# Kernel optimization log

Hardware: AMD Instinct MI355X
Metric: run time of the kernel (lower is better)

Reference implementation:

```python
import jax, jax.numpy as jnp
import numpy as np

EMBED_DIM = 512
N_QUERY = 4096
N_PROTO = 1024


def setup_inputs() -> dict:
    key = jax.random.key(0)
    k_q, k_p, k_wmu = jax.random.split(key, 3)
    d = EMBED_DIM
    bound = (6.0 / (d + d)) ** 0.5
    return {
        "query_features": jax.random.normal(k_q, (N_QUERY, d), dtype=jnp.float32),
        "prototypes": jax.random.normal(k_p, (N_PROTO, d), dtype=jnp.float32),
        "weight_mu": jax.random.uniform(k_wmu, (d, d), dtype=jnp.float32, minval=-bound, maxval=bound),
        "weight_rho": jnp.full((d, d), -3.0, dtype=jnp.float32),
        "bias_mu": jnp.zeros((d,), dtype=jnp.float32),
        "bias_rho": jnp.full((d,), 0.01, dtype=jnp.float32),
        "n_samples": 10,
    }


def reference(query_features, prototypes, weight_mu, weight_rho, bias_mu, bias_rho, n_samples):
    d = weight_mu.shape[0]
    # softplus reparameterization (same each iteration in the original loop)
    weight_sigma = jnp.log1p(jnp.exp(weight_rho))  # [d, d]
    bias_sigma = jnp.log1p(jnp.exp(bias_rho))      # [d]
    # batched MC weight/bias samples: [S, d, d] and [S, d]
    key = jax.random.key(42)
    kw, kb = jax.random.split(key)
    eps_w = jax.random.normal(kw, (n_samples, d, d), dtype=weight_mu.dtype)
    eps_b = jax.random.normal(kb, (n_samples, d), dtype=bias_mu.dtype)
    w = weight_mu[None] + weight_sigma[None] * eps_w   # [S, d, d]
    b = bias_mu[None] + bias_sigma[None] * eps_b       # [S, d]
    # F.linear(x, W_sample.T, b) == x @ W_sample + b
    tq = jnp.einsum('qd,sde->sqe', query_features, w) + b[:, None, :]  # [S, Q, d]
    # cdist via ||a||^2 + ||b||^2 - 2 a.b
    sq_q = jnp.sum(tq * tq, axis=-1)                    # [S, Q]
    sq_p = jnp.sum(prototypes * prototypes, axis=-1)    # [P]
    cross = jnp.einsum('sqe,pe->sqp', tq, prototypes)   # [S, Q, P]
    sqd = sq_q[:, :, None] + sq_p[None, None, :] - 2.0 * cross
    dists = jnp.sqrt(jnp.maximum(sqd, 1e-12))           # [S, Q, P]
    mean_distance = jnp.mean(dists, axis=0)
    uncertainty = jnp.std(dists, axis=0, ddof=1)        # torch.std is unbiased
    return mean_distance, uncertainty
```

## Files before the change

kernel.cpp:

```cpp
#include <hip/hip_runtime.h>
#include <stdint.h>

#define NS 10
#define DIM 512
#define NQ 4096
#define NP 1024

typedef unsigned short ushort_t;
typedef __bf16 bf16el_t;
typedef bf16el_t bf16x8 __attribute__((ext_vector_type(8)));
typedef float floatx4 __attribute__((ext_vector_type(4)));

__host__ __device__ __forceinline__ uint32_t rotl32(uint32_t x, int r) {
  return (x << r) | (x >> (32 - r));
}

__host__ __device__ __forceinline__ void threefry2x32(uint32_t k0, uint32_t k1,
                                                      uint32_t x0, uint32_t x1,
                                                      uint32_t* o0, uint32_t* o1) {
  uint32_t ks2 = k0 ^ k1 ^ 0x1BD11BDAu;
  x0 += k0; x1 += k1;
#define TF_R(r) { x0 += x1; x1 = rotl32(x1, r); x1 ^= x0; }
  TF_R(13) TF_R(15) TF_R(26) TF_R(6)   x0 += k1;  x1 += ks2 + 1u;
  TF_R(17) TF_R(29) TF_R(16) TF_R(24)  x0 += ks2; x1 += k0 + 2u;
  TF_R(13) TF_R(15) TF_R(26) TF_R(6)   x0 += k0;  x1 += k1 + 3u;
  TF_R(17) TF_R(29) TF_R(16) TF_R(24)  x0 += k1;  x1 += ks2 + 4u;
  TF_R(13) TF_R(15) TF_R(26) TF_R(6)   x0 += ks2; x1 += k0 + 5u;
#undef TF_R
  *o0 = x0; *o1 = x1;
}

__device__ __forceinline__ uint32_t jax_random_bits(uint32_t k0, uint32_t k1, uint32_t idx) {
  uint32_t o0, o1;
  threefry2x32(k0, k1, 0u, idx, &o0, &o1);
  return o0 ^ o1;
}

__device__ __forceinline__ float erfinvf_xla(float x) {
  float w = -log1pf(-x * x);
  float p;
  if (w < 5.0f) {
    w -= 2.5f;
    p = 2.81022636e-08f;
    p = fmaf(p, w, 3.43273939e-07f);
    p = fmaf(p, w, -3.5233877e-06f);
    p = fmaf(p, w, -4.39150654e-06f);
    p = fmaf(p, w, 0.00021858087f);
    p = fmaf(p, w, -0.00125372503f);
    p = fmaf(p, w, -0.00417768164f);
    p = fmaf(p, w, 0.246640727f);
    p = fmaf(p, w, 1.50140941f);
  } else {
    w = sqrtf(w) - 3.0f;
    p = -0.000200214257f;
    p = fmaf(p, w, 0.000100950558f);
    p = fmaf(p, w, 0.00134934322f);
    p = fmaf(p, w, -0.00367342844f);
    p = fmaf(p, w, 0.00573950773f);
    p = fmaf(p, w, -0.0076224613f);
    p = fmaf(p, w, 0.00943887047f);
    p = fmaf(p, w, 1.00167406f);
    p = fmaf(p, w, 2.83297682f);
  }
  return p * x;
}

__device__ __forceinline__ float jax_bits_to_normal(uint32_t bits) {
  float f = __uint_as_float((bits >> 9) | 0x3F800000u) - 1.0f;
  float u = f * 2.0f - 0.99999994f;
  u = fmaxf(u, -0.99999994f);
  return 1.41421356f * erfinvf_xla(u);
}

__device__ __forceinline__ float softplusf(float x) { return log1pf(expf(x)); }

__device__ __forceinline__ float bf2f(ushort_t u) {
  return __uint_as_float(((uint32_t)u) << 16);
}
__device__ __forceinline__ ushort_t f2bf(float f) {
  uint32_t u = __float_as_uint(f);
  u += 0x7FFFu + ((u >> 16) & 1u);
  return (ushort_t)(u >> 16);
}

__device__ __forceinline__ void gll16(const void* g, void* l) {
  __builtin_amdgcn_global_load_lds(
      (const __attribute__((address_space(1))) uint32_t*)g,
      (__attribute__((address_space(3))) uint32_t*)l, 16, 0, 0);
}

__global__ __launch_bounds__(256) void gen_w_kernel(const float* __restrict__ wmu,
                                                    const float* __restrict__ wrho,
                                                    ushort_t* __restrict__ wt,
                                                    uint32_t kw0, uint32_t kw1) {
  uint32_t tid = blockIdx.x * 256u + threadIdx.x;
  uint32_t s = tid >> 18;
  uint32_t r = tid & 0x3FFFFu;
  uint32_t e = r >> 9;
  uint32_t k = r & 511u;
  uint32_t eps_idx = (s << 18) | (k << 9) | e;
  uint32_t bits = jax_random_bits(kw0, kw1, eps_idx);
  float n = jax_bits_to_normal(bits);
  uint32_t mi = (k << 9) | e;
  float w = wmu[mi] + softplusf(wrho[mi]) * n;
  wt[tid] = f2bf(w);
}

__global__ __launch_bounds__(256) void prep_kernel(const float* __restrict__ qf,
                                                   const float* __restrict__ pf,
                                                   const float* __restrict__ bmu,
                                                   const float* __restrict__ brho,
                                                   ushort_t* __restrict__ qb,
                                                   ushort_t* __restrict__ pb,
                                                   float* __restrict__ sqp,
                                                   float* __restrict__ bvec,
                                                   float* __restrict__ sqq,
                                                   uint32_t kb0, uint32_t kb1) {
  const int blk = blockIdx.x;
  const int tid = threadIdx.x;
  if (blk < 2048) {
    int i = (blk * 256 + tid) * 4;
    float4 v = *(const float4*)&qf[i];
    uint2 r;
    r.x = (uint32_t)f2bf(v.x) | ((uint32_t)f2bf(v.y) << 16);
    r.y = (uint32_t)f2bf(v.z) | ((uint32_t)f2bf(v.w) << 16);
    *(uint2*)&qb[i] = r;
  } else if (blk < 2304) {
    int p = (blk - 2048) * 4 + (tid >> 6);
    int lane = tid & 63;
    const float* src = pf + p * DIM + lane * 8;
    float4 a = *(const float4*)src;
    float4 b = *(const float4*)(src + 4);
    float vals[8] = {a.x, a.y, a.z, a.w, b.x, b.y, b.z, b.w};
    ushort_t o[8];
    float ss = 0.f;
#pragma unroll
    for (int i = 0; i < 8; ++i) {
      o[i] = f2bf(vals[i]);
      float f = bf2f(o[i]);
      ss += f * f;
    }
    *(uint4*)&pb[p * DIM + lane * 8] = *(const uint4*)o;
#pragma unroll
    for (int off = 32; off; off >>= 1) ss += __shfl_xor(ss, off, 64);
    if (lane == 0) sqp[p] = ss;
  } else if (blk < 2324) {
    uint32_t t2 = (blk - 2304) * 256u + tid;
    uint32_t e = t2 & 511u;
    uint32_t bits = jax_random_bits(kb0, kb1, t2);
    float n = jax_bits_to_normal(bits);
    bvec[t2] = bmu[e] + softplusf(brho[e]) * n;
  } else {
    int i = (blk - 2324) * 256 + tid;
    sqq[i] = 0.f;
  }
}

__global__ __launch_bounds__(256) void gemm_tq_kernel(const ushort_t* __restrict__ qb,
                                                      const ushort_t* __restrict__ wt,
                                                      const float* __restrict__ bvec,
                                                      ushort_t* __restrict__ tq,
                                                      float* __restrict__ sqq) {
  __shared__ __align__(16) ushort_t ls[2 * 128 * 64];
  ushort_t* lsA = ls;
  ushort_t* lsB = ls + 128 * 64;
  const int lane = threadIdx.x & 63;
  const int wave = threadIdx.x >> 6;
  const int wm = wave >> 1, wn = wave & 1;
  const int qBase = blockIdx.x * 128;
  const int eBase = blockIdx.y * 128;
  const int s = blockIdx.z;
  const ushort_t* wbase = wt + (size_t)s * (DIM * DIM);
  const int srow = lane >> 3;
  const int scol = ((lane & 7) ^ srow) * 16;
  const char* gA = (const char*)qb + (size_t)(qBase + wave * 32 + srow) * (DIM * 2) + scol;
  const char* gB = (const char*)wbase + (size_t)(eBase + wave * 32 + srow) * (DIM * 2) + scol;
  char* lA = (char*)&lsA[wave * 32 * 64];
  char* lB = (char*)&lsB[wave * 32 * 64];
  const int cn = lane & 15;
  const int cn7 = cn & 7;
  const int jc = lane >> 4;
  const floatx4 fzero = {0.f, 0.f, 0.f, 0.f};
  floatx4 acc[4][4];
#pragma unroll
  for (int mi = 0; mi < 4; ++mi)
#pragma unroll
    for (int ni = 0; ni < 4; ++ni) acc[mi][ni] = fzero;

  for (int kt = 0; kt < 8; ++kt) {
    __syncthreads();
#pragma unroll
    for (int j = 0; j < 4; ++j) {
      gll16(gA + (size_t)j * 8 * (DIM * 2), lA + j * 1024);
      gll16(gB + (size_t)j * 8 * (DIM * 2), lB + j * 1024);
    }
    gA += 128; gB += 128;
    __syncthreads();
#pragma unroll
    for (int c = 0; c < 8; c += 4) {
      const int po = ((c + jc) ^ cn7) << 3;
      bf16x8 aF[4], bF[4];
#pragma unroll
      for (int mi = 0; mi < 4; ++mi)
        aF[mi] = *(const bf16x8*)&lsA[(wm * 64 + mi * 16 + cn) * 64 + po];
#pragma unroll
      for (int ni = 0; ni < 4; ++ni)
        bF[ni] = *(const bf16x8*)&lsB[(wn * 64 + ni * 16 + cn) * 64 + po];
#pragma unroll
      for (int mi = 0; mi < 4; ++mi)
#pragma unroll
        for (int ni = 0; ni < 4; ++ni)
          acc[mi][ni] = __builtin_amdgcn_mfma_f32_16x16x32_bf16(aF[mi], bF[ni], acc[mi][ni], 0, 0, 0);
    }
  }

  __syncthreads();
  ushort_t* area = ls + wave * 4096;
  float bv[4];
#pragma unroll
  for (int ni = 0; ni < 4; ++ni) bv[ni] = bvec[s * DIM + eBase + wn * 64 + ni * 16 + cn];
  const int jc4 = jc * 4;
#pragma unroll
  for (int mi = 0; mi < 4; ++mi)
#pragma unroll
    for (int ni = 0; ni < 4; ++ni)
#pragma unroll
      for (int r = 0; r < 4; ++r) {
        const int lr = mi * 16 + jc4 + r;
        const int lc = ni * 16 + cn;
        const int off = lr * 64 + (((lc >> 3) ^ (lr & 7)) << 3) + (lc & 7);
        area[off] = f2bf(acc[mi][ni][r] + bv[ni]);
      }
  __syncthreads();
  const int rr = lane >> 3;
  const int ch = lane & 7;
  const int physc = ch ^ rr;
  const size_t tqs = (size_t)s * (NQ * DIM);
#pragma unroll
  for (int pass = 0; pass < 8; ++pass) {
    const int lr = pass * 8 + rr;
    uint4 v = *(const uint4*)&area[lr * 64 + physc * 8];
    uint32_t wsv[4] = {v.x, v.y, v.z, v.w};
    float ss = 0.f;
#pragma unroll
    for (int i = 0; i < 4; ++i) {
      float lo = bf2f((ushort_t)(wsv[i] & 0xFFFFu));
      float hi = bf2f((ushort_t)(wsv[i] >> 16));
      ss += lo * lo + hi * hi;
    }
    ss += __shfl_xor(ss, 1, 64);
    ss += __shfl_xor(ss, 2, 64);
    ss += __shfl_xor(ss, 4, 64);
    const int q = qBase + wm * 64 + lr;
    *(uint4*)&tq[tqs + (size_t)q * DIM + eBase + wn * 64 + ch * 8] = v;
    if (ch == 0) atomicAdd(&sqq[s * NQ + q], ss);
  }
}

__global__ __launch_bounds__(256) void gemm_dist_kernel(const ushort_t* __restrict__ tq,
                                                        const ushort_t* __restrict__ pb,
                                                        const float* __restrict__ sqq,
                                                        const float* __restrict__ sqp,
                                                        float* __restrict__ out) {
  __shared__ __align__(16) ushort_t lsA[64 * 128];
  __shared__ __align__(16) ushort_t lsB[128 * 128];
  const int lane = threadIdx.x & 63;
  const int wave = threadIdx.x >> 6;
  const int wm = wave >> 1;
  const int wn = wave & 1;
  const int qBase = blockIdx.x * 64;
  const int pBase = blockIdx.y * 128;
  const int srow = lane >> 4;
  const int scc = lane & 15;
  const int sccx = scc ^ srow;
  const char* gA = (const char*)tq + (size_t)(qBase + wave * 16 + srow) * (DIM * 2);
  const char* gB = (const char*)pb + (size_t)(pBase + wave * 32 + srow) * (DIM * 2);
  char* lA = (char*)lsA + wave * 4096;
  char* lB = (char*)lsB + wave * 8192;
  const int cn = lane & 15;
  const int jc = lane >> 4;
  const int rq = jc * 4;
  const floatx4 fzero = {0.f, 0.f, 0.f, 0.f};

  float sum[2][4][4] = {};
  float ssq[2][4][4] = {};
  float sqp_v[4];
#pragma unroll
  for (int ni = 0; ni < 4; ++ni) sqp_v[ni] = sqp[pBase + wn * 64 + ni * 16 + cn];

  for (int s = 0; s < NS; ++s) {
    floatx4 acc[2][4];
#pragma unroll
    for (int mi = 0; mi < 2; ++mi)
#pragma unroll
      for (int ni = 0; ni < 4; ++ni) acc[mi][ni] = fzero;

    for (int kt = 0; kt < 4; ++kt) {
      __syncthreads();
#pragma unroll
      for (int g = 0; g < 4; ++g)
        gll16(gA + (size_t)g * 4 * (DIM * 2) + ((sccx ^ (g * 4)) << 4), lA + g * 1024);
#pragma unroll
      for (int g = 0; g < 8; ++g)
        gll16(gB + (size_t)g * 4 * (DIM * 2) + ((sccx ^ ((g & 3) * 4)) << 4), lB + g * 1024);
      gA += 256; gB += 256;
      __syncthreads();
#pragma unroll
      for (int c4 = 0; c4 < 4; ++c4) {
        const int po = (((c4 * 4 + jc) ^ cn) & 15) << 3;
        bf16x8 aF[2], bF[4];
#pragma unroll
        for (int mi = 0; mi < 2; ++mi)
          aF[mi] = *(const bf16x8*)&lsA[(wm * 32 + mi * 16 + cn) * 128 + po];
#pragma unroll
        for (int ni = 0; ni < 4; ++ni)
          bF[ni] = *(const bf16x8*)&lsB[(wn * 64 + ni * 16 + cn) * 128 + po];
#pragma unroll
        for (int mi = 0; mi < 2; ++mi)
#pragma unroll
          for (int ni = 0; ni < 4; ++ni)
            acc[mi][ni] = __builtin_amdgcn_mfma_f32_16x16x32_bf16(aF[mi], bF[ni], acc[mi][ni], 0, 0, 0);
      }
    }
    gA += (size_t)NQ * DIM * 2 - 1024;
    gB -= 1024;
#pragma unroll
    for (int mi = 0; mi < 2; ++mi) {
      float4 aqv = *(const float4*)&sqq[s * NQ + qBase + wm * 32 + mi * 16 + rq];
      float aqa[4] = {aqv.x, aqv.y, aqv.z, aqv.w};
#pragma unroll
      for (int r = 0; r < 4; ++r) {
        float aq = aqa[r];
#pragma unroll
        for (int ni = 0; ni < 4; ++ni) {
          float sqd = fmaxf(fmaf(-2.0f, acc[mi][ni][r], aq + sqp_v[ni]), 1e-12f);
          sum[mi][ni][r] += sqrtf(sqd);
          ssq[mi][ni][r] += sqd;
        }
      }
    }
  }
#pragma unroll
  for (int mi = 0; mi < 2; ++mi)
#pragma unroll
    for (int ni = 0; ni < 4; ++ni)
#pragma unroll
      for (int r = 0; r < 4; ++r) {
        int q = qBase + wm * 32 + mi * 16 + rq + r;
        int p = pBase + wn * 64 + ni * 16 + cn;
        float sm = sum[mi][ni][r];
        float mean = sm * 0.1f;
        float var = (ssq[mi][ni][r] - sm * sm * 0.1f) * (1.0f / 9.0f);
        out[(size_t)q * NP + p] = mean;
        out[(size_t)NQ * NP + (size_t)q * NP + p] = sqrtf(fmaxf(var, 0.0f));
      }
}

extern "C" void kernel_launch(void* const* d_in, const int* in_sizes, int n_in,
                              void* d_out, int out_size, void* d_ws, size_t ws_size,
                              hipStream_t stream) {
  const float* qf   = (const float*)d_in[0];
  const float* pf   = (const float*)d_in[1];
  const float* wmu  = (const float*)d_in[2];
  const float* wrho = (const float*)d_in[3];
  const float* bmu  = (const float*)d_in[4];
  const float* brho = (const float*)d_in[5];
  float* out = (float*)d_out;
  char* ws = (char*)d_ws;
  ushort_t* wt   = (ushort_t*)(ws);
  ushort_t* qb   = (ushort_t*)(ws + 5242880);
  ushort_t* pb   = (ushort_t*)(ws + 9437184);
  float*    bvec = (float*)   (ws + 10485760);
  float*    sqp  = (float*)   (ws + 10506240);
  ushort_t* tq   = (ushort_t*)(ws + 10510336);
  float*    sqq  = (float*)   (ws + 52453376);

  uint32_t kw0, kw1, kb0, kb1;
  threefry2x32(0u, 42u, 0u, 0u, &kw0, &kw1);
  threefry2x32(0u, 42u, 0u, 1u, &kb0, &kb1);

  hipLaunchKernelGGL(gen_w_kernel, dim3(10240), dim3(256), 0, stream, wmu, wrho, wt, kw0, kw1);
  hipLaunchKernelGGL(prep_kernel, dim3(2484), dim3(256), 0, stream,
                     qf, pf, bmu, brho, qb, pb, sqp, bvec, sqq, kb0, kb1);
  hipLaunchKernelGGL(gemm_tq_kernel, dim3(32, 4, 10), dim3(256), 0, stream, qb, wt, bvec, tq, sqq);
  hipLaunchKernelGGL(gemm_dist_kernel, dim3(64, 8), dim3(256), 0, stream, tq, pb, sqq, sqp, out);
}
```

Measured before the change: 210.3 us.

## Restructure distance GEMM to keep all samples' accumulators and reuse prototype tiles

The distance kernel now loops over K tiles on the outside and over the 10 samples on the inside. It keeps a 64x64 output tile's accumulators for every sample in registers, so the prototype fragments are loaded from LDS once per K tile and reused across all samples. Query tiles for the next sample are prefetched into a double-buffered LDS area while the current sample's MFMAs run. The grid doubles to 64x16 blocks with smaller 64-wide prototype tiles and launch_bounds(256,2). This raises register pressure (160 accumulator floats plus 16 B fragments per thread), which risks spills or lower occupancy.

New measurement: 223.3 us. +6.2%, slower.

```diff
diff --git a/kernel.cpp b/kernel.cpp
--- a/kernel.cpp
+++ b/kernel.cpp
@@ -257,103 +257,107 @@
   }
 }
 
-__global__ __launch_bounds__(256) void gemm_dist_kernel(const ushort_t* __restrict__ tq,
-                                                        const ushort_t* __restrict__ pb,
-                                                        const float* __restrict__ sqq,
-                                                        const float* __restrict__ sqp,
-                                                        float* __restrict__ out) {
-  __shared__ __align__(16) ushort_t lsA[64 * 128];
-  __shared__ __align__(16) ushort_t lsB[128 * 128];
+__global__ __launch_bounds__(256, 2) void gemm_dist_kernel(const ushort_t* __restrict__ tq,
+                                                           const ushort_t* __restrict__ pb,
+                                                           const float* __restrict__ sqq,
+                                                           const float* __restrict__ sqp,
+                                                           float* __restrict__ out) {
+  __shared__ __align__(16) ushort_t lsB[64 * 128];
+  __shared__ __align__(16) ushort_t lsA[2 * 64 * 128];
   const int lane = threadIdx.x & 63;
   const int wave = threadIdx.x >> 6;
-  const int wm = wave >> 1;
-  const int wn = wave & 1;
   const int qBase = blockIdx.x * 64;
-  const int pBase = blockIdx.y * 128;
-  const int srow = lane >> 4;
-  const int scc = lane & 15;
-  const int sccx = scc ^ srow;
-  const char* gA = (const char*)tq + (size_t)(qBase + wave * 16 + srow) * (DIM * 2);
-  const char* gB = (const char*)pb + (size_t)(pBase + wave * 32 + srow) * (DIM * 2);
-  char* lA = (char*)lsA + wave * 4096;
-  char* lB = (char*)lsB + wave * 8192;
+  const int pBase = blockIdx.y * 64;
   const int cn = lane & 15;
   const int jc = lane >> 4;
-  const int rq = jc * 4;
+  const int xorb = cn ^ jc;
+  const size_t aRowB = (size_t)(qBase + wave * 16 + jc) * (DIM * 2);
+  const size_t pRowB = (size_t)(pBase + wave * 16 + jc) * (DIM * 2);
+  const char* tqb = (const char*)tq;
+  const char* pbb = (const char*)pb;
+  char* lAb = (char*)lsA;
+  char* lBb = (char*)lsB;
+  int po[4];
+#pragma unroll
+  for (int c4 = 0; c4 < 4; ++c4) po[c4] = ((c4 * 4 + jc) ^ cn) << 3;
   const floatx4 fzero = {0.f, 0.f, 0.f, 0.f};
-
-  float sum[2][4][4] = {};
-  float ssq[2][4][4] = {};
-  float sqp_v[4];
-#pragma unroll
-  for (int ni = 0; ni < 4; ++ni) sqp_v[ni] = sqp[pBase + wn * 64 + ni * 16 + cn];
-
-  for (int s = 0; s < NS; ++s) {
-    floatx4 acc[2][4];
-#pragma unroll
-    for (int mi = 0; mi < 2; ++mi)
-#pragma unroll
-      for (int ni = 0; ni < 4; ++ni) acc[mi][ni] = fzero;
-
-    for (int kt = 0; kt < 4; ++kt) {
-      __syncthreads();
-#pragma unroll
-      for (int g = 0; g < 4; ++g)
-        gll16(gA + (size_t)g * 4 * (DIM * 2) + ((sccx ^ (g * 4)) << 4), lA + g * 1024);
-#pragma unroll
-      for (int g = 0; g < 8; ++g)
-        gll16(gB + (size_t)g * 4 * (DIM * 2) + ((sccx ^ ((g & 3) * 4)) << 4), lB + g * 1024);
-      gA += 256; gB += 256;
-      __syncthreads();
-#pragma unroll
-      for (int c4 = 0; c4 < 4; ++c4) {
-        const int po = (((c4 * 4 + jc) ^ cn) & 15) << 3;
-        bf16x8 aF[2], bF[4];
-#pragma unroll
-        for (int mi = 0; mi < 2; ++mi)
-          aF[mi] = *(const bf16x8*)&lsA[(wm * 32 + mi * 16 + cn) * 128 + po];
-#pragma unroll
-        for (int ni = 0; ni < 4; ++ni)
-          bF[ni] = *(const bf16x8*)&lsB[(wn * 64 + ni * 16 + cn) * 128 + po];
-#pragma unroll
-        for (int mi = 0; mi < 2; ++mi)
-#pragma unroll
-          for (int ni = 0; ni < 4; ++ni)
-            acc[mi][ni] = __builtin_amdgcn_mfma_f32_16x16x32_bf16(aF[mi], bF[ni], acc[mi][ni], 0, 0, 0);
-      }
-    }
-    gA += (size_t)NQ * DIM * 2 - 1024;
-    gB -= 1024;
-#pragma unroll
-    for (int mi = 0; mi < 2; ++mi) {
-      float4 aqv = *(const float4*)&sqq[s * NQ + qBase + wm * 32 + mi * 16 + rq];
-      float aqa[4] = {aqv.x, aqv.y, aqv.z, aqv.w};
-#pragma unroll
-      for (int r = 0; r < 4; ++r) {
-        float aq = aqa[r];
-#pragma unroll
-        for (int ni = 0; ni < 4; ++ni) {
-          float sqd = fmaxf(fmaf(-2.0f, acc[mi][ni][r], aq + sqp_v[ni]), 1e-12f);
-          sum[mi][ni][r] += sqrtf(sqd);
-          ssq[mi][ni][r] += sqd;
+  floatx4 acc[NS][4];
+#pragma unroll
+  for (int s = 0; s < NS; ++s)
+#pragma unroll
+    for (int ni = 0; ni < 4; ++ni) acc[s][ni] = fzero;
+
+  for (int kt = 0; kt < 4; ++kt) {
+    const size_t kOff = (size_t)kt * 256;
+#pragma unroll
+    for (int g = 0; g < 4; ++g) {
+      const size_t gRow = (size_t)g * 4 * (DIM * 2);
+      const size_t gSw = (size_t)((xorb ^ (g * 4)) << 4);
+      gll16(pbb + pRowB + gRow + gSw + kOff, lBb + wave * 4096 + g * 1024);
+      gll16(tqb + aRowB + gRow + gSw + kOff, lAb + wave * 4096 + g * 1024);
+    }
+    __syncthreads();
+    bf16x8 bFr[16];
+#pragma unroll
+    for (int c4 = 0; c4 < 4; ++c4)
+#pragma unroll
+      for (int ni = 0; ni < 4; ++ni)
+        bFr[c4 * 4 + ni] = *(const bf16x8*)&lsB[(ni * 16 + cn) * 128 + po[c4]];
+#pragma unroll
+    for (int s = 0; s < NS; ++s) {
+      if (s < NS - 1) {
+        char* dst = lAb + ((s + 1) & 1) * 16384 + wave * 4096;
+#pragma unroll
+        for (int g = 0; g < 4; ++g) {
+          const size_t gRow = (size_t)g * 4 * (DIM * 2);
+          const size_t gSw = (size_t)((xorb ^ (g * 4)) << 4);
+          gll16(tqb + (size_t)(s + 1) * (NQ * DIM * 2) + aRowB + gRow + gSw + kOff,
+                dst + g * 1024);
         }
       }
-    }
-  }
-#pragma unroll
-  for (int mi = 0; mi < 2; ++mi)
-#pragma unroll
-    for (int ni = 0; ni < 4; ++ni)
-#pragma unroll
-      for (int r = 0; r < 4; ++r) {
-        int q = qBase + wm * 32 + mi * 16 + rq + r;
-        int p = pBase + wn * 64 + ni * 16 + cn;
-        float sm = sum[mi][ni][r];
-        float mean = sm * 0.1f;
-        float var = (ssq[mi][ni][r] - sm * sm * 0.1f) * (1.0f / 9.0f);
-        out[(size_t)q * NP + p] = mean;
-        out[(size_t)NQ * NP + (size_t)q * NP + p] = sqrtf(fmaxf(var, 0.0f));
+      const ushort_t* aBuf = lsA + (s & 1) * 8192 + (wave * 16 + cn) * 128;
+#pragma unroll
+      for (int c4 = 0; c4 < 4; ++c4) {
+        bf16x8 aF = *(const bf16x8*)&aBuf[po[c4]];
+#pragma unroll
+        for (int ni = 0; ni < 4; ++ni)
+          acc[s][ni] = __builtin_amdgcn_mfma_f32_16x16x32_bf16(aF, bFr[c4 * 4 + ni], acc[s][ni], 0, 0, 0);
       }
+      __syncthreads();
+    }
+  }
+
+  float sqp_v[4];
+#pragma unroll
+  for (int ni = 0; ni < 4; ++ni) sqp_v[ni] = sqp[pBase + ni * 16 + cn];
+  float sum[4][4] = {};
+  float ssq[4][4] = {};
+#pragma unroll
+  for (int s = 0; s < NS; ++s) {
+    float4 aqv = *(const float4*)&sqq[s * NQ + qBase + wave * 16 + jc * 4];
+    float aqa[4] = {aqv.x, aqv.y, aqv.z, aqv.w};
+#pragma unroll
+    for (int r = 0; r < 4; ++r) {
+#pragma unroll
+      for (int ni = 0; ni < 4; ++ni) {
+        float sqd = fmaxf(fmaf(-2.0f, acc[s][ni][r], aqa[r] + sqp_v[ni]), 1e-12f);
+        sum[ni][r] += sqrtf(sqd);
+        ssq[ni][r] += sqd;
+      }
+    }
+  }
+#pragma unroll
+  for (int ni = 0; ni < 4; ++ni)
+#pragma unroll
+    for (int r = 0; r < 4; ++r) {
+      const int q = qBase + wave * 16 + jc * 4 + r;
+      const int p = pBase + ni * 16 + cn;
+      float sm = sum[ni][r];
+      float mean = sm * 0.1f;
+      float var = (ssq[ni][r] - sm * sm * 0.1f) * (1.0f / 9.0f);
+      out[(size_t)q * NP + p] = mean;
+      out[(size_t)NQ * NP + (size_t)q * NP + p] = sqrtf(fmaxf(var, 0.0f));
+    }
 }
 
 extern "C" void kernel_launch(void* const* d_in, const int* in_sizes, int n_in,
@@ -383,5 +387,5 @@
   hipLaunchKernelGGL(prep_kernel, dim3(2484), dim3(256), 0, stream,
                      qf, pf, bmu, brho, qb, pb, sqp, bvec, sqq, kb0, kb1);
   hipLaunchKernelGGL(gemm_tq_kernel, dim3(32, 4, 10), dim3(256), 0, stream, qb, wt, bvec, tq, sqq);
-  hipLaunchKernelGGL(gemm_dist_kernel, dim3(64, 8), dim3(256), 0, stream, tq, pb, sqq, sqp, out);
-}
+  hipLaunchKernelGGL(gemm_dist_kernel, dim3(64, 16), dim3(256), 0, stream, tq, pb, sqq, sqp, out);
+}
```

## Merge weight generation into prep kernel, share A tile across two samples, swap dist grid

Applied to the files above, without the earlier changes.

The separate weight-sampling kernel is folded into the prep kernel, saving one launch. The tq GEMM now computes two MC samples per block, so each query tile in LDS feeds two weight tiles, halving A-tile loads and the grid depth. This doubles accumulator registers and grows LDS to three tiles, which may cut occupancy. The distance GEMM grid is transposed so adjacent blocks share the same query rows, which may improve L2 reuse of tq.

New measurement: 237.7 us. 13.0% more time.

```diff
diff --git a/kernel.cpp b/kernel.cpp
--- a/kernel.cpp
+++ b/kernel.cpp
@@ -89,44 +89,43 @@
       (__attribute__((address_space(3))) uint32_t*)l, 16, 0, 0);
 }
 
-__global__ __launch_bounds__(256) void gen_w_kernel(const float* __restrict__ wmu,
-                                                    const float* __restrict__ wrho,
-                                                    ushort_t* __restrict__ wt,
-                                                    uint32_t kw0, uint32_t kw1) {
-  uint32_t tid = blockIdx.x * 256u + threadIdx.x;
-  uint32_t s = tid >> 18;
-  uint32_t r = tid & 0x3FFFFu;
-  uint32_t e = r >> 9;
-  uint32_t k = r & 511u;
-  uint32_t eps_idx = (s << 18) | (k << 9) | e;
-  uint32_t bits = jax_random_bits(kw0, kw1, eps_idx);
-  float n = jax_bits_to_normal(bits);
-  uint32_t mi = (k << 9) | e;
-  float w = wmu[mi] + softplusf(wrho[mi]) * n;
-  wt[tid] = f2bf(w);
-}
-
 __global__ __launch_bounds__(256) void prep_kernel(const float* __restrict__ qf,
                                                    const float* __restrict__ pf,
+                                                   const float* __restrict__ wmu,
+                                                   const float* __restrict__ wrho,
                                                    const float* __restrict__ bmu,
                                                    const float* __restrict__ brho,
+                                                   ushort_t* __restrict__ wt,
                                                    ushort_t* __restrict__ qb,
                                                    ushort_t* __restrict__ pb,
                                                    float* __restrict__ sqp,
                                                    float* __restrict__ bvec,
                                                    float* __restrict__ sqq,
+                                                   uint32_t kw0, uint32_t kw1,
                                                    uint32_t kb0, uint32_t kb1) {
   const int blk = blockIdx.x;
   const int tid = threadIdx.x;
-  if (blk < 2048) {
-    int i = (blk * 256 + tid) * 4;
+  if (blk < 10240) {
+    uint32_t t = blk * 256u + tid;
+    uint32_t s = t >> 18;
+    uint32_t r = t & 0x3FFFFu;
+    uint32_t e = r >> 9;
+    uint32_t k = r & 511u;
+    uint32_t eps_idx = (s << 18) | (k << 9) | e;
+    uint32_t bits = jax_random_bits(kw0, kw1, eps_idx);
+    float n = jax_bits_to_normal(bits);
+    uint32_t mi = (k << 9) | e;
+    float w = wmu[mi] + softplusf(wrho[mi]) * n;
+    wt[t] = f2bf(w);
+  } else if (blk < 12288) {
+    int i = ((blk - 10240) * 256 + tid) * 4;
     float4 v = *(const float4*)&qf[i];
     uint2 r;
     r.x = (uint32_t)f2bf(v.x) | ((uint32_t)f2bf(v.y) << 16);
     r.y = (uint32_t)f2bf(v.z) | ((uint32_t)f2bf(v.w) << 16);
     *(uint2*)&qb[i] = r;
-  } else if (blk < 2304) {
-    int p = (blk - 2048) * 4 + (tid >> 6);
+  } else if (blk < 12544) {
+    int p = (blk - 12288) * 4 + (tid >> 6);
     int lane = tid & 63;
     const float* src = pf + p * DIM + lane * 8;
     float4 a = *(const float4*)src;
@@ -144,14 +143,14 @@
 #pragma unroll
     for (int off = 32; off; off >>= 1) ss += __shfl_xor(ss, off, 64);
     if (lane == 0) sqp[p] = ss;
-  } else if (blk < 2324) {
-    uint32_t t2 = (blk - 2304) * 256u + tid;
+  } else if (blk < 12564) {
+    uint32_t t2 = (blk - 12544) * 256u + tid;
     uint32_t e = t2 & 511u;
     uint32_t bits = jax_random_bits(kb0, kb1, t2);
     float n = jax_bits_to_normal(bits);
     bvec[t2] = bmu[e] + softplusf(brho[e]) * n;
   } else {
-    int i = (blk - 2324) * 256 + tid;
+    int i = (blk - 12564) * 256 + tid;
     sqq[i] = 0.f;
   }
 }
@@ -161,99 +160,112 @@
                                                       const float* __restrict__ bvec,
                                                       ushort_t* __restrict__ tq,
                                                       float* __restrict__ sqq) {
-  __shared__ __align__(16) ushort_t ls[2 * 128 * 64];
+  __shared__ __align__(16) ushort_t ls[3 * 128 * 64];
   ushort_t* lsA = ls;
-  ushort_t* lsB = ls + 128 * 64;
   const int lane = threadIdx.x & 63;
   const int wave = threadIdx.x >> 6;
   const int wm = wave >> 1, wn = wave & 1;
   const int qBase = blockIdx.x * 128;
   const int eBase = blockIdx.y * 128;
-  const int s = blockIdx.z;
-  const ushort_t* wbase = wt + (size_t)s * (DIM * DIM);
+  const int s0 = blockIdx.z * 2;
   const int srow = lane >> 3;
   const int scol = ((lane & 7) ^ srow) * 16;
   const char* gA = (const char*)qb + (size_t)(qBase + wave * 32 + srow) * (DIM * 2) + scol;
-  const char* gB = (const char*)wbase + (size_t)(eBase + wave * 32 + srow) * (DIM * 2) + scol;
-  char* lA = (char*)&lsA[wave * 32 * 64];
-  char* lB = (char*)&lsB[wave * 32 * 64];
+  const char* gB0 = (const char*)(wt + (size_t)s0 * (DIM * DIM)) +
+                    (size_t)(eBase + wave * 32 + srow) * (DIM * 2) + scol;
+  const char* gB1 = gB0 + (size_t)(DIM * DIM) * 2;
+  char* lA = (char*)&ls[0 * 8192 + wave * 32 * 64];
+  char* lB0 = (char*)&ls[1 * 8192 + wave * 32 * 64];
+  char* lB1 = (char*)&ls[2 * 8192 + wave * 32 * 64];
   const int cn = lane & 15;
   const int cn7 = cn & 7;
   const int jc = lane >> 4;
   const floatx4 fzero = {0.f, 0.f, 0.f, 0.f};
-  floatx4 acc[4][4];
-#pragma unroll
-  for (int mi = 0; mi < 4; ++mi)
-#pragma unroll
-    for (int ni = 0; ni < 4; ++ni) acc[mi][ni] = fzero;
+  floatx4 acc[2][4][4];
+#pragma unroll
+  for (int sp = 0; sp < 2; ++sp)
+#pragma unroll
+    for (int mi = 0; mi < 4; ++mi)
+#pragma unroll
+      for (int ni = 0; ni < 4; ++ni) acc[sp][mi][ni] = fzero;
 
   for (int kt = 0; kt < 8; ++kt) {
     __syncthreads();
 #pragma unroll
     for (int j = 0; j < 4; ++j) {
       gll16(gA + (size_t)j * 8 * (DIM * 2), lA + j * 1024);
-      gll16(gB + (size_t)j * 8 * (DIM * 2), lB + j * 1024);
-    }
-    gA += 128; gB += 128;
+      gll16(gB0 + (size_t)j * 8 * (DIM * 2), lB0 + j * 1024);
+      gll16(gB1 + (size_t)j * 8 * (DIM * 2), lB1 + j * 1024);
+    }
+    gA += 128; gB0 += 128; gB1 += 128;
     __syncthreads();
 #pragma unroll
     for (int c = 0; c < 8; c += 4) {
       const int po = ((c + jc) ^ cn7) << 3;
-      bf16x8 aF[4], bF[4];
+      bf16x8 aF[4];
 #pragma unroll
       for (int mi = 0; mi < 4; ++mi)
-        aF[mi] = *(const bf16x8*)&lsA[(wm * 64 + mi * 16 + cn) * 64 + po];
-#pragma unroll
-      for (int ni = 0; ni < 4; ++ni)
-        bF[ni] = *(const bf16x8*)&lsB[(wn * 64 + ni * 16 + cn) * 64 + po];
-#pragma unroll
-      for (int mi = 0; mi < 4; ++mi)
+        aF[mi] = *(const bf16x8*)&ls[(wm * 64 + mi * 16 + cn) * 64 + po];
+#pragma unroll
+      for (int sp = 0; sp < 2; ++sp) {
+        bf16x8 bF[4];
 #pragma unroll
         for (int ni = 0; ni < 4; ++ni)
-          acc[mi][ni] = __builtin_amdgcn_mfma_f32_16x16x32_bf16(aF[mi], bF[ni], acc[mi][ni], 0, 0, 0);
-    }
-  }
-
-  __syncthreads();
-  ushort_t* area = ls + wave * 4096;
-  float bv[4];
-#pragma unroll
-  for (int ni = 0; ni < 4; ++ni) bv[ni] = bvec[s * DIM + eBase + wn * 64 + ni * 16 + cn];
+          bF[ni] = *(const bf16x8*)&ls[(1 + sp) * 8192 + (wn * 64 + ni * 16 + cn) * 64 + po];
+#pragma unroll
+        for (int mi = 0; mi < 4; ++mi)
+#pragma unroll
+          for (int ni = 0; ni < 4; ++ni)
+            acc[sp][mi][ni] =
+                __builtin_amdgcn_mfma_f32_16x16x32_bf16(aF[mi], bF[ni], acc[sp][mi][ni], 0, 0, 0);
+      }
+    }
+  }
+
   const int jc4 = jc * 4;
-#pragma unroll
-  for (int mi = 0; mi < 4; ++mi)
-#pragma unroll
-    for (int ni = 0; ni < 4; ++ni)
-#pragma unroll
-      for (int r = 0; r < 4; ++r) {
-        const int lr = mi * 16 + jc4 + r;
-        const int lc = ni * 16 + cn;
-        const int off = lr * 64 + (((lc >> 3) ^ (lr & 7)) << 3) + (lc & 7);
-        area[off] = f2bf(acc[mi][ni][r] + bv[ni]);
-      }
-  __syncthreads();
   const int rr = lane >> 3;
   const int ch = lane & 7;
   const int physc = ch ^ rr;
-  const size_t tqs = (size_t)s * (NQ * DIM);
-#pragma unroll
-  for (int pass = 0; pass < 8; ++pass) {
-    const int lr = pass * 8 + rr;
-    uint4 v = *(const uint4*)&area[lr * 64 + physc * 8];
-    uint32_t wsv[4] = {v.x, v.y, v.z, v.w};
-    float ss = 0.f;
-#pragma unroll
-    for (int i = 0; i < 4; ++i) {
-      float lo = bf2f((ushort_t)(wsv[i] & 0xFFFFu));
-      float hi = bf2f((ushort_t)(wsv[i] >> 16));
-      ss += lo * lo + hi * hi;
-    }
-    ss += __shfl_xor(ss, 1, 64);
-    ss += __shfl_xor(ss, 2, 64);
-    ss += __shfl_xor(ss, 4, 64);
-    const int q = qBase + wm * 64 + lr;
-    *(uint4*)&tq[tqs + (size_t)q * DIM + eBase + wn * 64 + ch * 8] = v;
-    if (ch == 0) atomicAdd(&sqq[s * NQ + q], ss);
+#pragma unroll
+  for (int sp = 0; sp < 2; ++sp) {
+    const int s = s0 + sp;
+    ushort_t* area = ls + wave * 4096;
+    float bv[4];
+#pragma unroll
+    for (int ni = 0; ni < 4; ++ni) bv[ni] = bvec[s * DIM + eBase + wn * 64 + ni * 16 + cn];
+    __syncthreads();
+#pragma unroll
+    for (int mi = 0; mi < 4; ++mi)
+#pragma unroll
+      for (int ni = 0; ni < 4; ++ni)
+#pragma unroll
+        for (int r = 0; r < 4; ++r) {
+          const int lr = mi * 16 + jc4 + r;
+          const int lc = ni * 16 + cn;
+          const int off = lr * 64 + (((lc >> 3) ^ (lr & 7)) << 3) + (lc & 7);
+          area[off] = f2bf(acc[sp][mi][ni][r] + bv[ni]);
+        }
+    __syncthreads();
+    const size_t tqs = (size_t)s * (NQ * DIM);
+#pragma unroll
+    for (int pass = 0; pass < 8; ++pass) {
+      const int lr = pass * 8 + rr;
+      uint4 v = *(const uint4*)&area[lr * 64 + physc * 8];
+      uint32_t wsv[4] = {v.x, v.y, v.z, v.w};
+      float ss = 0.f;
+#pragma unroll
+      for (int i = 0; i < 4; ++i) {
+        float lo = bf2f((ushort_t)(wsv[i] & 0xFFFFu));
+        float hi = bf2f((ushort_t)(wsv[i] >> 16));
+        ss += lo * lo + hi * hi;
+      }
+      ss += __shfl_xor(ss, 1, 64);
+      ss += __shfl_xor(ss, 2, 64);
+      ss += __shfl_xor(ss, 4, 64);
+      const int q = qBase + wm * 64 + lr;
+      *(uint4*)&tq[tqs + (size_t)q * DIM + eBase + wn * 64 + ch * 8] = v;
+      if (ch == 0) atomicAdd(&sqq[s * NQ + q], ss);
+    }
   }
 }
 
@@ -268,8 +280,8 @@
   const int wave = threadIdx.x >> 6;
   const int wm = wave >> 1;
   const int wn = wave & 1;
-  const int qBase = blockIdx.x * 64;
-  const int pBase = blockIdx.y * 128;
+  const int qBase = blockIdx.y * 64;
+  const int pBase = blockIdx.x * 128;
   const int srow = lane >> 4;
   const int scc = lane & 15;
   const int sccx = scc ^ srow;
@@ -379,9 +391,9 @@
   threefry2x32(0u, 42u, 0u, 0u, &kw0, &kw1);
   threefry2x32(0u, 42u, 0u, 1u, &kb0, &kb1);
 
-  hipLaunchKernelGGL(gen_w_kernel, dim3(10240), dim3(256), 0, stream, wmu, wrho, wt, kw0, kw1);
-  hipLaunchKernelGGL(prep_kernel, dim3(2484), dim3(256), 0, stream,
-                     qf, pf, bmu, brho, qb, pb, sqp, bvec, sqq, kb0, kb1);
-  hipLaunchKernelGGL(gemm_tq_kernel, dim3(32, 4, 10), dim3(256), 0, stream, qb, wt, bvec, tq, sqq);
-  hipLaunchKernelGGL(gemm_dist_kernel, dim3(64, 8), dim3(256), 0, stream, tq, pb, sqq, sqp, out);
-}
+  hipLaunchKernelGGL(prep_kernel, dim3(12724), dim3(256), 0, stream,
+                     qf, pf, wmu, wrho, bmu, brho, wt, qb, pb, sqp, bvec, sqq,
+                     kw0, kw1, kb0, kb1);
+  hipLaunchKernelGGL(gemm_tq_kernel, dim3(32, 4, 5), dim3(256), 0, stream, qb, wt, bvec, tq, sqq);
+  hipLaunchKernelGGL(gemm_dist_kernel, dim3(8, 64), dim3(256), 0, stream, tq, pb, sqq, sqp, out);
+}
```
